# Optimization experiments

Hardware: AMD Instinct MI355X
Metric: run time of the kernel (lower is better)

Reference implementation:

```python
import jax, jax.numpy as jnp
import numpy as np

B, S, HID = 2, 2048, 1024
H, HKV, D = 8, 2, 256
G = H // HKV            # GQA group size = 4
RD = D // 4             # partial rotary dim = 64
BASE = 10000000.0
EPS = 1e-6


def _rmsnorm(x, w):
    # x: [..., D]; matches QwenRMSNorm (fp32 math)
    xf = x.astype(jnp.float32)
    var = jnp.mean(xf * xf, axis=-1, keepdims=True)
    return w * (xf * jax.lax.rsqrt(var + EPS)).astype(x.dtype)


def _rotate_half(x):
    h = x.shape[-1] // 2
    return jnp.concatenate([-x[..., h:], x[..., :h]], axis=-1)


def _rope_cos_sin(position_ids, dtype):
    inv_freq = 1.0 / (BASE ** (jnp.arange(0, RD, 2, dtype=jnp.float32) / RD))
    freqs = position_ids.astype(jnp.float32)[:, None] * inv_freq[None, :]  # [S, RD/2]
    emb = jnp.concatenate([freqs, freqs], axis=-1)                          # [S, RD]
    return jnp.cos(emb).astype(dtype)[None, None], jnp.sin(emb).astype(dtype)[None, None]


def setup_inputs() -> dict:
    key = jax.random.key(0)
    ks = jax.random.split(key, 8)
    sc = lambda fan_in: 1.0 / np.sqrt(fan_in)
    return {
        "hidden_states": jax.random.normal(ks[0], (B, S, HID), jnp.float32),
        "position_ids": jnp.arange(S, dtype=jnp.int32),
        "Wq": jax.random.normal(ks[1], (H * D * 2, HID), jnp.float32) * sc(HID),
        "Wk": jax.random.normal(ks[2], (HKV * D, HID), jnp.float32) * sc(HID),
        "Wv": jax.random.normal(ks[3], (HKV * D, HID), jnp.float32) * sc(HID),
        "Wo": jax.random.normal(ks[4], (HID, H * D), jnp.float32) * sc(H * D),
        "q_norm_w": jnp.ones((D,), jnp.float32),
        "k_norm_w": jnp.ones((D,), jnp.float32),
    }


def reference(hidden_states, position_ids, Wq, Wk, Wv, Wo, q_norm_w, k_norm_w):
    b, s, _ = hidden_states.shape
    q_and_gate = hidden_states @ Wq.T                      # [B,S,2*H*D]
    q = q_and_gate[..., : H * D]
    gate = q_and_gate[..., H * D :]
    k = hidden_states @ Wk.T                               # [B,S,HKV*D]
    v = hidden_states @ Wv.T

    q = _rmsnorm(q.reshape(b, s, H, D), q_norm_w).transpose(0, 2, 1, 3)    # [B,H,S,D]
    k = _rmsnorm(k.reshape(b, s, HKV, D), k_norm_w).transpose(0, 2, 1, 3)  # [B,HKV,S,D]
    v = v.reshape(b, s, HKV, D).transpose(0, 2, 1, 3)                       # [B,HKV,S,D]

    cos, sin = _rope_cos_sin(position_ids, q.dtype)        # [1,1,S,RD]
    q_rot, q_pass = q[..., :RD], q[..., RD:]
    k_rot, k_pass = k[..., :RD], k[..., RD:]
    q = jnp.concatenate([q_rot * cos + _rotate_half(q_rot) * sin, q_pass], axis=-1)
    k = jnp.concatenate([k_rot * cos + _rotate_half(k_rot) * sin, k_pass], axis=-1)

    # GQA: group q heads by kv head instead of repeat_interleave (same math)
    qg = q.reshape(b, HKV, G, s, D)
    scale = 1.0 / np.sqrt(D).astype(np.float32)
    scores = jnp.einsum('bhgqd,bhkd->bhgqk', qg, k) * scale  # [B,HKV,G,S,S]
    attn = jax.nn.softmax(scores, axis=-1)                   # NOTE: no causal mask (as in source)
    out = jnp.einsum('bhgqk,bhkd->bhgqd', attn, v)           # [B,HKV,G,S,D]
    out = out.reshape(b, H, s, D).transpose(0, 2, 1, 3).reshape(b, s, H * D)

    out = out * jax.nn.silu(gate)
    return out @ Wo.T
```

## Files before the change

### kernel.cpp

```cpp
#include <hip/hip_runtime.h>
#include <math.h>

typedef unsigned short u16;
typedef unsigned int   u32;
typedef __attribute__((ext_vector_type(4))) float f32x4;
typedef __attribute__((ext_vector_type(8))) short s16x8;
typedef __attribute__((ext_vector_type(4))) unsigned short u16x4;

#define B_N   2
#define S_N   2048
#define HID_N 1024
#define H_N   8
#define HKV_N 2
#define D_N   256
#define QKVW  5120

__device__ __forceinline__ u16 f2bf(float f) {
  union { float f; u32 u; } x; x.f = f;
  u32 r = x.u + 0x7FFFu + ((x.u >> 16) & 1u);
  return (u16)(r >> 16);
}
__device__ __forceinline__ float bf2f(u16 u) {
  union { u32 u; float f; } x; x.u = ((u32)u) << 16; return x.f;
}
__device__ __forceinline__ u32 pk_bf16(float lo, float hi) {
  u32 r;
  asm("v_cvt_pk_bf16_f32 %0, %1, %2" : "=v"(r) : "v"(lo), "v"(hi));
  return r;
}
__device__ __forceinline__ void gload_lds16(const u16* g, u16* l) {
  __builtin_amdgcn_global_load_lds((const __attribute__((address_space(1))) u32*)g,
                                   (__attribute__((address_space(3))) u32*)l, 16, 0, 0);
}

#define N4_HS 1048576
#define N4_WQ 1048576
#define N4_WK 131072
#define N4_WV 131072
#define N4_WO 524288
#define N4_TOT (N4_HS + N4_WQ + N4_WK + N4_WV + N4_WO)

__global__ __launch_bounds__(256)
void cast5_kernel(const float* __restrict__ hs, const float* __restrict__ wq,
                  const float* __restrict__ wk, const float* __restrict__ wv,
                  const float* __restrict__ wo, u16* __restrict__ hs_bf,
                  u16* __restrict__ wqkv_bf, u16* __restrict__ wo_bf) {
  int i = blockIdx.x * blockDim.x + threadIdx.x;
  const int stride = gridDim.x * blockDim.x;
  for (; i < N4_TOT; i += stride) {
    const float* src; u16* dst; int k;
    if (i < N4_HS)                         { src = hs; dst = hs_bf; k = i; }
    else if (i < N4_HS + N4_WQ)            { src = wq; dst = wqkv_bf; k = i - N4_HS; }
    else if (i < N4_HS + N4_WQ + N4_WK)    { src = wk; dst = wqkv_bf + 4194304; k = i - (N4_HS + N4_WQ); }
    else if (i < N4_TOT - N4_WO)           { src = wv; dst = wqkv_bf + 4718592; k = i - (N4_HS + N4_WQ + N4_WK); }
    else                                   { src = wo; dst = wo_bf; k = i - (N4_TOT - N4_WO); }
    float4 v = reinterpret_cast<const float4*>(src)[k];
    u16x4 o;
    o.x = f2bf(v.x); o.y = f2bf(v.y); o.z = f2bf(v.z); o.w = f2bf(v.w);
    reinterpret_cast<u16x4*>(dst)[k] = o;
  }
}

__global__ __launch_bounds__(256)
void trig_kernel(const int* __restrict__ pos, float* __restrict__ ct, float* __restrict__ st) {
  int i = blockIdx.x * blockDim.x + threadIdx.x;
  if (i >= S_N * 32) return;
  int s = i >> 5, j = i & 31;
  double inv = exp(-(double)j * (log(1.0e7) / 32.0));
  double ang = (double)pos[s] * inv;
  ct[i] = (float)cos(ang);
  st[i] = (float)sin(ang);
}

template <int OUT_BF16>
__global__ __launch_bounds__(256, 2)
void gemm_bt_kernel(const u16* __restrict__ A, const u16* __restrict__ Bw,
                    void* __restrict__ Cout, int M, int N, int K, int bn_per_x) {
  const int x = blockIdx.x & 7;
  const int i0 = blockIdx.x >> 3;
  const int bm = i0 / bn_per_x;
  const int bn = x * bn_per_x + (i0 - bm * bn_per_x);
  const int tid = threadIdx.x;
  const int lane = tid & 63;
  const int wr = tid >> 7;
  const int wc = (tid >> 6) & 1;
  __shared__ u16 sA[2][128 * 64];
  __shared__ u16 sB[2][128 * 64];
  f32x4 acc[4][4] = {};
  const u16* Ab = A + (size_t)(bm << 7) * K;
  const u16* Bb = Bw + (size_t)(bn << 7) * K;
  const int nkt = K >> 6;

  auto stage = [&](int buf, int kt) {
    const int k0 = kt << 6;
#pragma unroll
    for (int i = 0; i < 4; ++i) {
      const int L = i * 256 + tid;
      const int r = L >> 3, s = L & 7;
      gload_lds16(Ab + (size_t)r * K + k0 + ((s ^ (r & 7)) << 3), &sA[buf][L * 8]);
    }
#pragma unroll
    for (int i = 0; i < 4; ++i) {
      const int L = i * 256 + tid;
      const int r = L >> 3, s = L & 7;
      gload_lds16(Bb + (size_t)r * K + k0 + ((s ^ (r & 7)) << 3), &sB[buf][L * 8]);
    }
  };

  stage(0, 0);
  int cur = 0;
  const int ra = (wr << 6) + (lane & 15);
  const int rb = (wc << 6) + (lane & 15);
  const int l4 = (lane >> 4);
  const int sw = lane & 7;
  for (int kt = 0; kt < nkt; ++kt) {
    if (kt + 1 < nkt) {
      stage(cur ^ 1, kt + 1);
      asm volatile("s_waitcnt vmcnt(8)" ::: "memory");
    } else {
      asm volatile("s_waitcnt vmcnt(0)" ::: "memory");
    }
    __builtin_amdgcn_s_barrier();
    const u16* sa = sA[cur];
    const u16* sb = sB[cur];
#pragma unroll
    for (int kk = 0; kk < 2; ++kk) {
      const int sl = ((kk * 4 + l4) ^ sw) << 3;
      s16x8 af[4], bfr[4];
#pragma unroll
      for (int m = 0; m < 4; ++m)
        af[m] = *reinterpret_cast<const s16x8*>(sa + (ra + m * 16) * 64 + sl);
#pragma unroll
      for (int n = 0; n < 4; ++n)
        bfr[n] = *reinterpret_cast<const s16x8*>(sb + (rb + n * 16) * 64 + sl);
#pragma unroll
      for (int m = 0; m < 4; ++m)
#pragma unroll
        for (int n = 0; n < 4; ++n)
          acc[m][n] = __builtin_amdgcn_mfma_f32_16x16x32_bf16(af[m], bfr[n], acc[m][n], 0, 0, 0);
    }
    __builtin_amdgcn_s_barrier();
    cur ^= 1;
  }
  const int row0 = (bm << 7) + (wr << 6) + ((lane >> 4) << 2);
  const int col0 = (bn << 7) + (wc << 6) + (lane & 15);
#pragma unroll
  for (int m = 0; m < 4; ++m)
#pragma unroll
    for (int n = 0; n < 4; ++n)
#pragma unroll
      for (int j = 0; j < 4; ++j) {
        size_t idx = (size_t)(row0 + m * 16 + j) * N + col0 + n * 16;
        if (OUT_BF16) ((u16*)Cout)[idx] = f2bf(acc[m][n][j]);
        else          ((float*)Cout)[idx] = acc[m][n][j];
      }
}

__global__ __launch_bounds__(256)
void normrope_kernel(const u16* __restrict__ qkv, const float* __restrict__ qw,
                     const float* __restrict__ kw, const float* __restrict__ ct,
                     const float* __restrict__ st, u16* __restrict__ q_r,
                     u16* __restrict__ k_r) {
  const int lane = threadIdx.x & 63;
  const int row = blockIdx.x * 4 + (threadIdx.x >> 6);
  const int nq = B_N * S_N * H_N;
  const u16* src; u16* dst; const float* w;
  int s;
  if (row < nq) {
    int h = row & 7; int bs = row >> 3; s = bs & (S_N - 1); int b = bs >> 11;
    src = qkv + (size_t)(b * S_N + s) * QKVW + h * 256;
    dst = q_r + ((size_t)(b * H_N + h) * S_N + s) * 256;
    w = qw;
  } else {
    int r2 = row - nq;
    int h = r2 & 1; int bs = r2 >> 1; s = bs & (S_N - 1); int b = bs >> 11;
    src = qkv + (size_t)(b * S_N + s) * QKVW + 4096 + h * 256;
    dst = k_r + ((size_t)(b * HKV_N + h) * S_N + s) * 256;
    w = kw;
  }
  u16x4 xv = *reinterpret_cast<const u16x4*>(src + lane * 4);
  float x0 = bf2f(xv.x), x1 = bf2f(xv.y), x2 = bf2f(xv.z), x3 = bf2f(xv.w);
  float ss = x0 * x0 + x1 * x1 + x2 * x2 + x3 * x3;
#pragma unroll
  for (int off = 1; off < 64; off <<= 1) ss += __shfl_xor(ss, off);
  float rinv = rsqrtf(ss * (1.0f / 256.0f) + 1e-6f);
  float4 wv = *reinterpret_cast<const float4*>(w + lane * 4);
  float y[4] = { x0 * rinv * wv.x, x1 * rinv * wv.y, x2 * rinv * wv.z, x3 * rinv * wv.w };
  float p[4];
  p[0] = __shfl_xor(y[0], 8);
  p[1] = __shfl_xor(y[1], 8);
  p[2] = __shfl_xor(y[2], 8);
  p[3] = __shfl_xor(y[3], 8);
  if (lane < 16) {
    const float sgn = (lane < 8) ? -1.0f : 1.0f;
    const int jb = (lane * 4) & 31;
#pragma unroll
    for (int e = 0; e < 4; ++e) {
      float c = ct[(size_t)s * 32 + jb + e];
      float sn = st[(size_t)s * 32 + jb + e];
      y[e] = y[e] * c + sgn * p[e] * sn;
    }
  }
  u16x4 ov;
  ov.x = f2bf(y[0]); ov.y = f2bf(y[1]); ov.z = f2bf(y[2]); ov.w = f2bf(y[3]);
  *reinterpret_cast<u16x4*>(dst + lane * 4) = ov;
}

__global__ __launch_bounds__(256)
void vtrans_kernel(const u16* __restrict__ qkv, u16* __restrict__ vt) {
  const int bid = blockIdx.x;
  const int dt = bid & 3;
  const int stile = (bid >> 2) & 31;
  const int bh = bid >> 7;
  const int b = bh >> 1, kvh = bh & 1;
  __shared__ u16 tile[64][68];
  const int t = threadIdx.x;
  const u16* src = qkv + (size_t)(b * S_N + stile * 64) * QKVW + 4608 + kvh * 256 + dt * 64;
#pragma unroll
  for (int i = 0; i < 2; ++i) {
    int sl = i * 32 + (t >> 3);
    int d8 = (t & 7) * 8;
    s16x8 v = *reinterpret_cast<const s16x8*>(src + (size_t)sl * QKVW + d8);
    u16x4 lo = { (u16)v[0], (u16)v[1], (u16)v[2], (u16)v[3] };
    u16x4 hi = { (u16)v[4], (u16)v[5], (u16)v[6], (u16)v[7] };
    *reinterpret_cast<u16x4*>(&tile[sl][d8]) = lo;
    *reinterpret_cast<u16x4*>(&tile[sl][d8 + 4]) = hi;
  }
  __syncthreads();
#pragma unroll
  for (int i = 0; i < 2; ++i) {
    int dl = i * 32 + (t >> 3);
    int s8 = (t & 7) * 8;
    u16 tmp[8];
#pragma unroll
    for (int e = 0; e < 8; ++e) tmp[e] = tile[s8 + e][dl];
    u16x4 lo = { tmp[0], tmp[1], tmp[2], tmp[3] };
    u16x4 hi = { tmp[4], tmp[5], tmp[6], tmp[7] };
    u16* dstp = vt + ((size_t)(bh * 256 + dt * 64 + dl)) * S_N + stile * 64 + s8;
    *reinterpret_cast<u16x4*>(dstp) = lo;
    *reinterpret_cast<u16x4*>(dstp + 4) = hi;
  }
}

__global__ __launch_bounds__(512, 2)
void attn_kernel(const u16* __restrict__ q_r, const u16* __restrict__ k_r,
                 const u16* __restrict__ vt, const u16* __restrict__ qkv,
                 u16* __restrict__ act) {
  const int dd = blockIdx.x;
  const int xcd = dd & 7;
  const int idx = dd >> 3;
  const int combo = xcd >> 1;
  const int within = (xcd & 1) * 32 + idx;
  const int b = combo >> 1;
  const int kvh = combo & 1;
  const int h = kvh * 4 + (within >> 4);
  const int qt = within & 15;

  const int tid = threadIdx.x;
  const int lane = tid & 63;
  const int wv = tid >> 6;
  const int l15 = lane & 15;
  const int l4 = lane >> 4;

  __shared__ u16 sK[2][64 * 256];
  __shared__ u16 sVt[2][256 * 64];
  __shared__ u16 sP[8][16 * 64];

  const int q0 = qt * 128 + wv * 16;
  const u16* qb = q_r + ((size_t)(b * H_N + h) * S_N + q0) * 256;
  s16x8 qf[8];
#pragma unroll
  for (int kk = 0; kk < 8; ++kk)
    qf[kk] = *reinterpret_cast<const s16x8*>(qb + (size_t)l15 * 256 + kk * 32 + l4 * 8);

  f32x4 oacc[16] = {};
  float mrow = -1e30f;
  float lrow = 0.f;

  const u16* kbase = k_r + ((size_t)(b * HKV_N + kvh) * S_N) * 256;
  const u16* vbase = vt + ((size_t)(b * HKV_N + kvh) * 256) * S_N;

  const int krow_b = tid >> 5;
  const int kp = tid & 31;
  const int vrow_b = tid >> 3;
  const int vp = tid & 7;

  auto stageKV = [&](int buf, int step) {
    const int kv0 = step << 6;
#pragma unroll
    for (int i = 0; i < 4; ++i) {
      const int krow = i * 16 + krow_b;
      gload_lds16(kbase + (size_t)(kv0 + krow) * 256 + ((kp ^ (krow_b & 7)) << 3),
                  &sK[buf][i * 4096 + tid * 8]);
    }
#pragma unroll
    for (int i = 0; i < 4; ++i) {
      const int vrow = i * 64 + vrow_b;
      gload_lds16(vbase + (size_t)vrow * S_N + kv0 + ((vp ^ (vrow_b & 7)) << 3),
                  &sVt[buf][i * 4096 + tid * 8]);
    }
  };

  stageKV(0, 0);
  int cur = 0;
  const float scale = 0.0625f;
  const int sw = l15 & 7;
  const int swp = l15 & 14;
  for (int step = 0; step < 32; ++step) {
    asm volatile("s_waitcnt vmcnt(0)" ::: "memory");
    __builtin_amdgcn_s_barrier();
    if (step + 1 < 32) stageKV(cur ^ 1, step + 1);
    const u16* ktile = sK[cur];
    const u16* vtile = sVt[cur];

    f32x4 sacc[4] = {};
#pragma unroll
    for (int kk = 0; kk < 8; ++kk) {
      const int slot = kk * 4 + l4;
#pragma unroll
      for (int g = 0; g < 4; ++g) {
        s16x8 kf = *reinterpret_cast<const s16x8*>(
            ktile + (g * 16 + l15) * 256 + ((slot ^ sw) << 3));
        sacc[g] = __builtin_amdgcn_mfma_f32_16x16x32_bf16(kf, qf[kk], sacc[g], 0, 0, 0);
      }
    }

    float vmax = sacc[0][0];
#pragma unroll
    for (int g = 0; g < 4; ++g)
#pragma unroll
      for (int j = 0; j < 4; ++j) vmax = fmaxf(vmax, sacc[g][j]);
    vmax = fmaxf(vmax, __shfl_xor(vmax, 16));
    vmax = fmaxf(vmax, __shfl_xor(vmax, 32));
    if (__any(vmax > mrow)) {
      float mnew = fmaxf(mrow, vmax);
      float alpha = __expf((mrow - mnew) * scale);
      mrow = mnew;
      lrow *= alpha;
      float ab[4];
#pragma unroll
      for (int j = 0; j < 4; ++j) ab[j] = __shfl(alpha, l4 * 4 + j);
#pragma unroll
      for (int nf = 0; nf < 16; ++nf) {
        oacc[nf][0] *= ab[0]; oacc[nf][1] *= ab[1];
        oacc[nf][2] *= ab[2]; oacc[nf][3] *= ab[3];
      }
    }
    const float msc = mrow * scale;
    float p[16];
#pragma unroll
    for (int g = 0; g < 4; ++g)
#pragma unroll
      for (int j = 0; j < 4; ++j)
        p[g * 4 + j] = __expf(fmaf(sacc[g][j], scale, -msc));
    float r = ((p[0] + p[1]) + (p[2] + p[3])) + ((p[4] + p[5]) + (p[6] + p[7]))
            + ((p[8] + p[9]) + (p[10] + p[11])) + ((p[12] + p[13]) + (p[14] + p[15]));
    r += __shfl_xor(r, 16);
    r += __shfl_xor(r, 32);
    lrow += r;

    u16* pl = &sP[wv][0];
#pragma unroll
    for (int g = 0; g < 4; ++g) {
      u32 lo = pk_bf16(p[g * 4 + 0], p[g * 4 + 1]);
      u32 hi = pk_bf16(p[g * 4 + 2], p[g * 4 + 3]);
      union { u32 w[2]; u16x4 v; } u;
      u.w[0] = lo; u.w[1] = hi;
      *reinterpret_cast<u16x4*>(pl + l15 * 64 + (((g * 4 + l4) ^ swp) << 2)) = u.v;
    }
    asm volatile("s_waitcnt lgkmcnt(0)" ::: "memory");
    __builtin_amdgcn_sched_barrier(0);

#pragma unroll
    for (int c = 0; c < 2; ++c) {
      s16x8 paf = *reinterpret_cast<const s16x8*>(
          pl + l15 * 64 + (((c * 8 + l4 * 2) ^ swp) << 2));
#pragma unroll
      for (int nf = 0; nf < 16; ++nf) {
        s16x8 vf = *reinterpret_cast<const s16x8*>(
            vtile + (nf * 16 + l15) * 64 + (((c * 4 + l4) ^ sw) << 3));
        oacc[nf] = __builtin_amdgcn_mfma_f32_16x16x32_bf16(paf, vf, oacc[nf], 0, 0, 0);
      }
    }
    cur ^= 1;
  }

  float invl = 1.0f / lrow;
  float ib[4];
#pragma unroll
  for (int j = 0; j < 4; ++j) ib[j] = __shfl(invl, l4 * 4 + j);
#pragma unroll
  for (int nf = 0; nf < 16; ++nf) {
#pragma unroll
    for (int j = 0; j < 4; ++j) {
      const int srow = q0 + l4 * 4 + j;
      const int d = nf * 16 + l15;
      float o = oacc[nf][j] * ib[j];
      float g = bf2f(qkv[(size_t)(b * S_N + srow) * QKVW + 2048 + h * 256 + d]);
      float sg = g / (1.0f + __expf(-g));
      act[(size_t)(b * S_N + srow) * 2048 + h * 256 + d] = f2bf(o * sg);
    }
  }
}

extern "C" void kernel_launch(void* const* d_in, const int* in_sizes, int n_in,
                              void* d_out, int out_size, void* d_ws, size_t ws_size,
                              hipStream_t stream) {
  const float* hs  = (const float*)d_in[0];
  const int*   pos = (const int*)d_in[1];
  const float* Wq  = (const float*)d_in[2];
  const float* Wk  = (const float*)d_in[3];
  const float* Wv  = (const float*)d_in[4];
  const float* Wo  = (const float*)d_in[5];
  const float* qw  = (const float*)d_in[6];
  const float* kw  = (const float*)d_in[7];
  float* out = (float*)d_out;

  char* w8 = (char*)d_ws;
  u16* hs_bf   = (u16*)(w8);
  u16* wqkv_bf = (u16*)(w8 + 8388608);
  u16* wo_bf   = (u16*)(w8 + 18874368);
  u16* qkv_raw = (u16*)(w8 + 23068672);
  u16* q_r     = (u16*)(w8 + 65011712);
  u16* k_r     = (u16*)(w8 + 81788928);
  u16* vt      = (u16*)(w8 + 85983232);
  u16* act     = (u16*)(w8 + 90177536);
  float* cost  = (float*)(w8 + 106954752);
  float* sint  = (float*)(w8 + 107216896);

  cast5_kernel<<<2048, 256, 0, stream>>>(hs, Wq, Wk, Wv, Wo, hs_bf, wqkv_bf, wo_bf);

  trig_kernel<<<(S_N * 32) / 256, 256, 0, stream>>>(pos, cost, sint);

  gemm_bt_kernel<1><<<1280, 256, 0, stream>>>(hs_bf, wqkv_bf, (void*)qkv_raw,
                                              4096, 5120, 1024, 5);

  normrope_kernel<<<(B_N * S_N * (H_N + HKV_N)) / 4, 256, 0, stream>>>(
      qkv_raw, qw, kw, cost, sint, q_r, k_r);
  vtrans_kernel<<<512, 256, 0, stream>>>(qkv_raw, vt);

  attn_kernel<<<256, 512, 0, stream>>>(q_r, k_r, vt, qkv_raw, act);

  gemm_bt_kernel<0><<<256, 256, 0, stream>>>(act, wo_bf, (void*)out,
                                             4096, 1024, 2048, 1);
}
```

Baseline: 220.8 us.

## Share K/V tiles across GQA heads and split KV range between wave groups

Result: slower. 244.6 us (+10.8%).

```diff
diff --git a/kernel.cpp b/kernel.cpp
--- a/kernel.cpp
+++ b/kernel.cpp
@@ -250,54 +250,60 @@
   const int xcd = dd & 7;
   const int idx = dd >> 3;
   const int combo = xcd >> 1;
-  const int within = (xcd & 1) * 32 + idx;
+  const int qt = (xcd & 1) * 32 + idx;
   const int b = combo >> 1;
   const int kvh = combo & 1;
-  const int h = kvh * 4 + (within >> 4);
-  const int qt = within & 15;
 
   const int tid = threadIdx.x;
   const int lane = tid & 63;
   const int wv = tid >> 6;
+  const int grp = wv >> 2;
+  const int hw = wv & 3;
+  const int h = kvh * 4 + hw;
   const int l15 = lane & 15;
   const int l4 = lane >> 4;
 
-  __shared__ u16 sK[2][64 * 256];
-  __shared__ u16 sVt[2][256 * 64];
-  __shared__ u16 sP[8][16 * 64];
-
-  const int q0 = qt * 128 + wv * 16;
+  __shared__ u16 smem[74752];
+  u16* sKg = smem + grp * 16384;
+  u16* sVg = smem + 32768 + grp * 16384;
+  u16* sPw = smem + 65536 + wv * 1024;
+  float* sml = (float*)(smem + 73728);
+
+  const int q0 = qt * 32;
   const u16* qb = q_r + ((size_t)(b * H_N + h) * S_N + q0) * 256;
-  s16x8 qf[8];
-#pragma unroll
-  for (int kk = 0; kk < 8; ++kk)
-    qf[kk] = *reinterpret_cast<const s16x8*>(qb + (size_t)l15 * 256 + kk * 32 + l4 * 8);
-
-  f32x4 oacc[16] = {};
-  float mrow = -1e30f;
-  float lrow = 0.f;
+  s16x8 qf[2][8];
+#pragma unroll
+  for (int rg = 0; rg < 2; ++rg)
+#pragma unroll
+    for (int kk = 0; kk < 8; ++kk)
+      qf[rg][kk] = *reinterpret_cast<const s16x8*>(
+          qb + (size_t)(rg * 16 + l15) * 256 + kk * 32 + l4 * 8);
+
+  f32x4 oacc[2][16] = {};
+  float mrow[2] = { -1e30f, -1e30f };
+  float lrow[2] = { 0.f, 0.f };
 
   const u16* kbase = k_r + ((size_t)(b * HKV_N + kvh) * S_N) * 256;
   const u16* vbase = vt + ((size_t)(b * HKV_N + kvh) * 256) * S_N;
-
-  const int krow_b = tid >> 5;
-  const int kp = tid & 31;
-  const int vrow_b = tid >> 3;
-  const int vp = tid & 7;
+  const int gt = tid & 255;
 
   auto stageKV = [&](int buf, int step) {
-    const int kv0 = step << 6;
+    const int kv0 = grp * 1024 + (step << 5);
+    u16* kb = sKg + buf * 8192;
+    u16* vb = sVg + buf * 8192;
 #pragma unroll
     for (int i = 0; i < 4; ++i) {
-      const int krow = i * 16 + krow_b;
-      gload_lds16(kbase + (size_t)(kv0 + krow) * 256 + ((kp ^ (krow_b & 7)) << 3),
-                  &sK[buf][i * 4096 + tid * 8]);
+      const int L = i * 256 + gt;
+      const int krow = L >> 5, ks = L & 31;
+      gload_lds16(kbase + (size_t)(kv0 + krow) * 256 + ((ks ^ (krow & 7)) << 3),
+                  kb + L * 8);
     }
 #pragma unroll
     for (int i = 0; i < 4; ++i) {
-      const int vrow = i * 64 + vrow_b;
-      gload_lds16(vbase + (size_t)vrow * S_N + kv0 + ((vp ^ (vrow_b & 7)) << 3),
-                  &sVt[buf][i * 4096 + tid * 8]);
+      const int L = i * 256 + gt;
+      const int vrow = L >> 2, vs = L & 3;
+      gload_lds16(vbase + (size_t)vrow * S_N + kv0 + ((vs ^ (vrow & 3)) << 3),
+                  vb + L * 8);
     }
   };
 
@@ -305,101 +311,161 @@
   int cur = 0;
   const float scale = 0.0625f;
   const int sw = l15 & 7;
-  const int swp = l15 & 14;
+  const int sw3 = l15 & 3;
   for (int step = 0; step < 32; ++step) {
     asm volatile("s_waitcnt vmcnt(0)" ::: "memory");
     __builtin_amdgcn_s_barrier();
     if (step + 1 < 32) stageKV(cur ^ 1, step + 1);
-    const u16* ktile = sK[cur];
-    const u16* vtile = sVt[cur];
-
-    f32x4 sacc[4] = {};
+    const u16* ktile = sKg + cur * 8192;
+    const u16* vtile = sVg + cur * 8192;
+
+    f32x4 sacc[2][2] = {};
 #pragma unroll
     for (int kk = 0; kk < 8; ++kk) {
       const int slot = kk * 4 + l4;
 #pragma unroll
-      for (int g = 0; g < 4; ++g) {
+      for (int g = 0; g < 2; ++g) {
         s16x8 kf = *reinterpret_cast<const s16x8*>(
             ktile + (g * 16 + l15) * 256 + ((slot ^ sw) << 3));
-        sacc[g] = __builtin_amdgcn_mfma_f32_16x16x32_bf16(kf, qf[kk], sacc[g], 0, 0, 0);
+        sacc[0][g] = __builtin_amdgcn_mfma_f32_16x16x32_bf16(kf, qf[0][kk], sacc[0][g], 0, 0, 0);
+        sacc[1][g] = __builtin_amdgcn_mfma_f32_16x16x32_bf16(kf, qf[1][kk], sacc[1][g], 0, 0, 0);
       }
     }
 
-    float vmax = sacc[0][0];
-#pragma unroll
-    for (int g = 0; g < 4; ++g)
-#pragma unroll
-      for (int j = 0; j < 4; ++j) vmax = fmaxf(vmax, sacc[g][j]);
-    vmax = fmaxf(vmax, __shfl_xor(vmax, 16));
-    vmax = fmaxf(vmax, __shfl_xor(vmax, 32));
-    if (__any(vmax > mrow)) {
-      float mnew = fmaxf(mrow, vmax);
-      float alpha = __expf((mrow - mnew) * scale);
-      mrow = mnew;
-      lrow *= alpha;
-      float ab[4];
-#pragma unroll
-      for (int j = 0; j < 4; ++j) ab[j] = __shfl(alpha, l4 * 4 + j);
-#pragma unroll
-      for (int nf = 0; nf < 16; ++nf) {
-        oacc[nf][0] *= ab[0]; oacc[nf][1] *= ab[1];
-        oacc[nf][2] *= ab[2]; oacc[nf][3] *= ab[3];
+    float vmax[2];
+#pragma unroll
+    for (int rg = 0; rg < 2; ++rg) {
+      float v = fmaxf(fmaxf(fmaxf(sacc[rg][0][0], sacc[rg][0][1]),
+                            fmaxf(sacc[rg][0][2], sacc[rg][0][3])),
+                      fmaxf(fmaxf(sacc[rg][1][0], sacc[rg][1][1]),
+                            fmaxf(sacc[rg][1][2], sacc[rg][1][3])));
+      v = fmaxf(v, __shfl_xor(v, 16));
+      v = fmaxf(v, __shfl_xor(v, 32));
+      vmax[rg] = v;
+    }
+    if (__any(fmaxf(vmax[0] - mrow[0], vmax[1] - mrow[1]) > 0.0f)) {
+      float alpha[2];
+#pragma unroll
+      for (int rg = 0; rg < 2; ++rg) {
+        float mnew = fmaxf(mrow[rg], vmax[rg]);
+        alpha[rg] = __expf((mrow[rg] - mnew) * scale);
+        mrow[rg] = mnew;
+        lrow[rg] *= alpha[rg];
       }
-    }
-    const float msc = mrow * scale;
-    float p[16];
-#pragma unroll
-    for (int g = 0; g < 4; ++g)
-#pragma unroll
-      for (int j = 0; j < 4; ++j)
-        p[g * 4 + j] = __expf(fmaf(sacc[g][j], scale, -msc));
-    float r = ((p[0] + p[1]) + (p[2] + p[3])) + ((p[4] + p[5]) + (p[6] + p[7]))
-            + ((p[8] + p[9]) + (p[10] + p[11])) + ((p[12] + p[13]) + (p[14] + p[15]));
-    r += __shfl_xor(r, 16);
-    r += __shfl_xor(r, 32);
-    lrow += r;
-
-    u16* pl = &sP[wv][0];
-#pragma unroll
-    for (int g = 0; g < 4; ++g) {
-      u32 lo = pk_bf16(p[g * 4 + 0], p[g * 4 + 1]);
-      u32 hi = pk_bf16(p[g * 4 + 2], p[g * 4 + 3]);
-      union { u32 w[2]; u16x4 v; } u;
-      u.w[0] = lo; u.w[1] = hi;
-      *reinterpret_cast<u16x4*>(pl + l15 * 64 + (((g * 4 + l4) ^ swp) << 2)) = u.v;
+      float ab[2][4];
+#pragma unroll
+      for (int rg = 0; rg < 2; ++rg)
+#pragma unroll
+        for (int j = 0; j < 4; ++j) ab[rg][j] = __shfl(alpha[rg], l4 * 4 + j);
+#pragma unroll
+      for (int nf = 0; nf < 16; ++nf)
+#pragma unroll
+        for (int rg = 0; rg < 2; ++rg) {
+          oacc[rg][nf][0] *= ab[rg][0]; oacc[rg][nf][1] *= ab[rg][1];
+          oacc[rg][nf][2] *= ab[rg][2]; oacc[rg][nf][3] *= ab[rg][3];
+        }
+    }
+    float p[2][8];
+#pragma unroll
+    for (int rg = 0; rg < 2; ++rg) {
+      const float msc = mrow[rg] * scale;
+#pragma unroll
+      for (int g = 0; g < 2; ++g)
+#pragma unroll
+        for (int j = 0; j < 4; ++j)
+          p[rg][g * 4 + j] = __expf(fmaf(sacc[rg][g][j], scale, -msc));
+      float r = ((p[rg][0] + p[rg][1]) + (p[rg][2] + p[rg][3]))
+              + ((p[rg][4] + p[rg][5]) + (p[rg][6] + p[rg][7]));
+      r += __shfl_xor(r, 16);
+      r += __shfl_xor(r, 32);
+      lrow[rg] += r;
+    }
+
+#pragma unroll
+    for (int rg = 0; rg < 2; ++rg) {
+      const int rowoff = (rg * 16 + l15) * 32;
+#pragma unroll
+      for (int g = 0; g < 2; ++g) {
+        u32 a = pk_bf16(p[rg][g * 4 + 0], p[rg][g * 4 + 1]);
+        u32 c = pk_bf16(p[rg][g * 4 + 2], p[rg][g * 4 + 3]);
+        union { u32 w[2]; u16x4 v; } u;
+        u.w[0] = a; u.w[1] = c;
+        *reinterpret_cast<u16x4*>(
+            sPw + rowoff + (((g * 2 + (l4 >> 1)) ^ sw3) << 3) + ((l4 & 1) << 2)) = u.v;
+      }
     }
     asm volatile("s_waitcnt lgkmcnt(0)" ::: "memory");
     __builtin_amdgcn_sched_barrier(0);
 
-#pragma unroll
-    for (int c = 0; c < 2; ++c) {
-      s16x8 paf = *reinterpret_cast<const s16x8*>(
-          pl + l15 * 64 + (((c * 8 + l4 * 2) ^ swp) << 2));
-#pragma unroll
-      for (int nf = 0; nf < 16; ++nf) {
-        s16x8 vf = *reinterpret_cast<const s16x8*>(
-            vtile + (nf * 16 + l15) * 64 + (((c * 4 + l4) ^ sw) << 3));
-        oacc[nf] = __builtin_amdgcn_mfma_f32_16x16x32_bf16(paf, vf, oacc[nf], 0, 0, 0);
+    s16x8 paf[2];
+#pragma unroll
+    for (int rg = 0; rg < 2; ++rg)
+      paf[rg] = *reinterpret_cast<const s16x8*>(
+          sPw + (rg * 16 + l15) * 32 + ((l4 ^ sw3) << 3));
+#pragma unroll
+    for (int nf = 0; nf < 16; ++nf) {
+      s16x8 vf = *reinterpret_cast<const s16x8*>(
+          vtile + (nf * 16 + l15) * 32 + ((l4 ^ sw3) << 3));
+      oacc[0][nf] = __builtin_amdgcn_mfma_f32_16x16x32_bf16(paf[0], vf, oacc[0][nf], 0, 0, 0);
+      oacc[1][nf] = __builtin_amdgcn_mfma_f32_16x16x32_bf16(paf[1], vf, oacc[1][nf], 0, 0, 0);
+    }
+    cur ^= 1;
+  }
+
+  __syncthreads();
+  if (l4 == 0) {
+    sml[wv * 64 + l15 * 2]            = mrow[0];
+    sml[wv * 64 + l15 * 2 + 1]        = lrow[0];
+    sml[wv * 64 + (16 + l15) * 2]     = mrow[1];
+    sml[wv * 64 + (16 + l15) * 2 + 1] = lrow[1];
+  }
+  float* mergeO = (float*)smem;
+  if (grp == 1) {
+#pragma unroll
+    for (int rg = 0; rg < 2; ++rg)
+#pragma unroll
+      for (int nf = 0; nf < 16; ++nf)
+#pragma unroll
+        for (int j = 0; j < 4; ++j) {
+          const int q = rg * 16 + l4 * 4 + j;
+          const int d = nf * 16 + l15;
+          mergeO[(hw * 32 + q) * 260 + d] = oacc[rg][nf][j];
+        }
+  }
+  __syncthreads();
+  if (grp == 0) {
+    float W0[2][4], W1[2][4];
+#pragma unroll
+    for (int rg = 0; rg < 2; ++rg)
+#pragma unroll
+      for (int j = 0; j < 4; ++j) {
+        const int q = rg * 16 + l4 * 4 + j;
+        const float m0 = sml[hw * 64 + q * 2];
+        const float l0 = sml[hw * 64 + q * 2 + 1];
+        const float m1 = sml[(4 + hw) * 64 + q * 2];
+        const float l1 = sml[(4 + hw) * 64 + q * 2 + 1];
+        const float M = fmaxf(m0, m1);
+        const float w0 = __expf((m0 - M) * scale);
+        const float w1 = __expf((m1 - M) * scale);
+        const float inv = 1.0f / (l0 * w0 + l1 * w1);
+        W0[rg][j] = w0 * inv;
+        W1[rg][j] = w1 * inv;
       }
-    }
-    cur ^= 1;
-  }
-
-  float invl = 1.0f / lrow;
-  float ib[4];
-#pragma unroll
-  for (int j = 0; j < 4; ++j) ib[j] = __shfl(invl, l4 * 4 + j);
-#pragma unroll
-  for (int nf = 0; nf < 16; ++nf) {
-#pragma unroll
-    for (int j = 0; j < 4; ++j) {
-      const int srow = q0 + l4 * 4 + j;
-      const int d = nf * 16 + l15;
-      float o = oacc[nf][j] * ib[j];
-      float g = bf2f(qkv[(size_t)(b * S_N + srow) * QKVW + 2048 + h * 256 + d]);
-      float sg = g / (1.0f + __expf(-g));
-      act[(size_t)(b * S_N + srow) * 2048 + h * 256 + d] = f2bf(o * sg);
-    }
+#pragma unroll
+    for (int rg = 0; rg < 2; ++rg)
+#pragma unroll
+      for (int nf = 0; nf < 16; ++nf)
+#pragma unroll
+        for (int j = 0; j < 4; ++j) {
+          const int q = rg * 16 + l4 * 4 + j;
+          const int d = nf * 16 + l15;
+          const int srow = q0 + q;
+          float o = oacc[rg][nf][j] * W0[rg][j]
+                  + mergeO[(hw * 32 + q) * 260 + d] * W1[rg][j];
+          float g = bf2f(qkv[(size_t)(b * S_N + srow) * QKVW + 2048 + h * 256 + d]);
+          float sg = g / (1.0f + __expf(-g));
+          act[(size_t)(b * S_N + srow) * 2048 + h * 256 + d] = f2bf(o * sg);
+        }
   }
 }
 
```

## Software-pipeline attention loop to overlap next QK with current PV

Applied to the files above, without the earlier changes.

Result: no change. 219.5 us, median of 3 (-0.6%).

```diff
diff --git a/kernel.cpp b/kernel.cpp
--- a/kernel.cpp
+++ b/kernel.cpp
@@ -264,7 +264,7 @@
 
   __shared__ u16 sK[2][64 * 256];
   __shared__ u16 sVt[2][256 * 64];
-  __shared__ u16 sP[8][16 * 64];
+  __shared__ u16 sP[8][2][16 * 64];
 
   const int q0 = qt * 128 + wv * 16;
   const u16* qb = q_r + ((size_t)(b * H_N + h) * S_N + q0) * 256;
@@ -285,7 +285,7 @@
   const int vrow_b = tid >> 3;
   const int vp = tid & 7;
 
-  auto stageKV = [&](int buf, int step) {
+  auto stageK = [&](int buf, int step) {
     const int kv0 = step << 6;
 #pragma unroll
     for (int i = 0; i < 4; ++i) {
@@ -293,6 +293,9 @@
       gload_lds16(kbase + (size_t)(kv0 + krow) * 256 + ((kp ^ (krow_b & 7)) << 3),
                   &sK[buf][i * 4096 + tid * 8]);
     }
+  };
+  auto stageV = [&](int buf, int step) {
+    const int kv0 = step << 6;
 #pragma unroll
     for (int i = 0; i < 4; ++i) {
       const int vrow = i * 64 + vrow_b;
@@ -301,19 +304,11 @@
     }
   };
 
-  stageKV(0, 0);
-  int cur = 0;
   const float scale = 0.0625f;
   const int sw = l15 & 7;
   const int swp = l15 & 14;
-  for (int step = 0; step < 32; ++step) {
-    asm volatile("s_waitcnt vmcnt(0)" ::: "memory");
-    __builtin_amdgcn_s_barrier();
-    if (step + 1 < 32) stageKV(cur ^ 1, step + 1);
-    const u16* ktile = sK[cur];
-    const u16* vtile = sVt[cur];
-
-    f32x4 sacc[4] = {};
+
+  auto computeQK = [&](const u16* ktile, f32x4* sacc) {
 #pragma unroll
     for (int kk = 0; kk < 8; ++kk) {
       const int slot = kk * 4 + l4;
@@ -324,7 +319,10 @@
         sacc[g] = __builtin_amdgcn_mfma_f32_16x16x32_bf16(kf, qf[kk], sacc[g], 0, 0, 0);
       }
     }
-
+  };
+  float alphaNext = 1.0f;
+  int doRescale = 0;
+  auto softmaxPack = [&](f32x4* sacc, int pb) {
     float vmax = sacc[0][0];
 #pragma unroll
     for (int g = 0; g < 4; ++g)
@@ -332,19 +330,14 @@
       for (int j = 0; j < 4; ++j) vmax = fmaxf(vmax, sacc[g][j]);
     vmax = fmaxf(vmax, __shfl_xor(vmax, 16));
     vmax = fmaxf(vmax, __shfl_xor(vmax, 32));
-    if (__any(vmax > mrow)) {
+    doRescale = __any(vmax > mrow) ? 1 : 0;
+    if (doRescale) {
       float mnew = fmaxf(mrow, vmax);
-      float alpha = __expf((mrow - mnew) * scale);
+      alphaNext = __expf((mrow - mnew) * scale);
       mrow = mnew;
-      lrow *= alpha;
-      float ab[4];
-#pragma unroll
-      for (int j = 0; j < 4; ++j) ab[j] = __shfl(alpha, l4 * 4 + j);
-#pragma unroll
-      for (int nf = 0; nf < 16; ++nf) {
-        oacc[nf][0] *= ab[0]; oacc[nf][1] *= ab[1];
-        oacc[nf][2] *= ab[2]; oacc[nf][3] *= ab[3];
-      }
+      lrow *= alphaNext;
+    } else {
+      alphaNext = 1.0f;
     }
     const float msc = mrow * scale;
     float p[16];
@@ -358,8 +351,7 @@
     r += __shfl_xor(r, 16);
     r += __shfl_xor(r, 32);
     lrow += r;
-
-    u16* pl = &sP[wv][0];
+    u16* pl = &sP[wv][pb][0];
 #pragma unroll
     for (int g = 0; g < 4; ++g) {
       u32 lo = pk_bf16(p[g * 4 + 0], p[g * 4 + 1]);
@@ -368,9 +360,39 @@
       u.w[0] = lo; u.w[1] = hi;
       *reinterpret_cast<u16x4*>(pl + l15 * 64 + (((g * 4 + l4) ^ swp) << 2)) = u.v;
     }
-    asm volatile("s_waitcnt lgkmcnt(0)" ::: "memory");
-    __builtin_amdgcn_sched_barrier(0);
-
+  };
+
+  stageK(0, 0);
+  stageV(0, 0);
+  stageK(1, 1);
+  asm volatile("s_waitcnt vmcnt(0)" ::: "memory");
+  __builtin_amdgcn_s_barrier();
+  {
+    f32x4 sacc[4] = {};
+    computeQK(sK[0], sacc);
+    softmaxPack(sacc, 0);
+  }
+
+  for (int t = 0; t < 32; ++t) {
+    asm volatile("s_waitcnt vmcnt(0)" ::: "memory");
+    __builtin_amdgcn_s_barrier();
+    if (t + 2 < 32) stageK(t & 1, t + 2);
+    if (t + 1 < 32) stageV((t + 1) & 1, t + 1);
+
+    if (doRescale) {
+      float ab[4];
+#pragma unroll
+      for (int j = 0; j < 4; ++j) ab[j] = __shfl(alphaNext, l4 * 4 + j);
+#pragma unroll
+      for (int nf = 0; nf < 16; ++nf) {
+        oacc[nf][0] *= ab[0]; oacc[nf][1] *= ab[1];
+        oacc[nf][2] *= ab[2]; oacc[nf][3] *= ab[3];
+      }
+    }
+
+    __builtin_amdgcn_s_setprio(1);
+    const u16* pl = &sP[wv][t & 1][0];
+    const u16* vtile = sVt[t & 1];
 #pragma unroll
     for (int c = 0; c < 2; ++c) {
       s16x8 paf = *reinterpret_cast<const s16x8*>(
@@ -382,7 +404,11 @@
         oacc[nf] = __builtin_amdgcn_mfma_f32_16x16x32_bf16(paf, vf, oacc[nf], 0, 0, 0);
       }
     }
-    cur ^= 1;
+    f32x4 sacc[4] = {};
+    if (t + 1 < 32) computeQK(sK[(t + 1) & 1], sacc);
+    __builtin_amdgcn_s_setprio(0);
+
+    if (t + 1 < 32) softmaxPack(sacc, (t + 1) & 1);
   }
 
   float invl = 1.0f / lrow;
```

## Split attention KV range across wave pairs with 32x32 MFMA and merge partials

Applied to the files above, without the earlier changes.

Result: slower. 367.4 us (+66.4%).

```diff
diff --git a/kernel.cpp b/kernel.cpp
--- a/kernel.cpp
+++ b/kernel.cpp
@@ -4,6 +4,7 @@
 typedef unsigned short u16;
 typedef unsigned int   u32;
 typedef __attribute__((ext_vector_type(4))) float f32x4;
+typedef __attribute__((ext_vector_type(16))) float f32x16;
 typedef __attribute__((ext_vector_type(8))) short s16x8;
 typedef __attribute__((ext_vector_type(4))) unsigned short u16x4;
 
@@ -242,7 +243,7 @@
   }
 }
 
-__global__ __launch_bounds__(512, 2)
+__global__ __launch_bounds__(256, 2)
 void attn_kernel(const u16* __restrict__ q_r, const u16* __restrict__ k_r,
                  const u16* __restrict__ vt, const u16* __restrict__ qkv,
                  u16* __restrict__ act) {
@@ -250,155 +251,173 @@
   const int xcd = dd & 7;
   const int idx = dd >> 3;
   const int combo = xcd >> 1;
-  const int within = (xcd & 1) * 32 + idx;
+  const int within = (xcd & 1) * 64 + idx;
   const int b = combo >> 1;
   const int kvh = combo & 1;
-  const int h = kvh * 4 + (within >> 4);
-  const int qt = within & 15;
+  const int h = kvh * 4 + (within >> 5);
+  const int qtile = within & 31;
 
   const int tid = threadIdx.x;
   const int lane = tid & 63;
-  const int wv = tid >> 6;
-  const int l15 = lane & 15;
-  const int l4 = lane >> 4;
-
-  __shared__ u16 sK[2][64 * 256];
-  __shared__ u16 sVt[2][256 * 64];
-  __shared__ u16 sP[8][16 * 64];
-
-  const int q0 = qt * 128 + wv * 16;
+  const int w = tid >> 6;
+  const int half = w >> 1;
+  const int l31 = lane & 31;
+  const int l5 = lane >> 5;
+
+  __shared__ u16 smem[36864];
+  u16* sK = smem + half * 8192;
+  u16* sV = smem + 16384 + half * 8192;
+  u16* sP = smem + 32768 + w * 1024;
+
+  const int q0 = qtile * 64 + (w & 1) * 32;
   const u16* qb = q_r + ((size_t)(b * H_N + h) * S_N + q0) * 256;
-  s16x8 qf[8];
-#pragma unroll
-  for (int kk = 0; kk < 8; ++kk)
-    qf[kk] = *reinterpret_cast<const s16x8*>(qb + (size_t)l15 * 256 + kk * 32 + l4 * 8);
-
-  f32x4 oacc[16] = {};
-  float mrow = -1e30f;
-  float lrow = 0.f;
-
-  const u16* kbase = k_r + ((size_t)(b * HKV_N + kvh) * S_N) * 256;
-  const u16* vbase = vt + ((size_t)(b * HKV_N + kvh) * 256) * S_N;
-
-  const int krow_b = tid >> 5;
-  const int kp = tid & 31;
-  const int vrow_b = tid >> 3;
-  const int vp = tid & 7;
-
-  auto stageKV = [&](int buf, int step) {
-    const int kv0 = step << 6;
-#pragma unroll
-    for (int i = 0; i < 4; ++i) {
-      const int krow = i * 16 + krow_b;
-      gload_lds16(kbase + (size_t)(kv0 + krow) * 256 + ((kp ^ (krow_b & 7)) << 3),
-                  &sK[buf][i * 4096 + tid * 8]);
-    }
-#pragma unroll
-    for (int i = 0; i < 4; ++i) {
-      const int vrow = i * 64 + vrow_b;
-      gload_lds16(vbase + (size_t)vrow * S_N + kv0 + ((vp ^ (vrow_b & 7)) << 3),
-                  &sVt[buf][i * 4096 + tid * 8]);
+  s16x8 qf[16];
+#pragma unroll
+  for (int ks = 0; ks < 16; ++ks)
+    qf[ks] = *reinterpret_cast<const s16x8*>(qb + (size_t)l31 * 256 + ks * 16 + l5 * 8);
+
+  f32x16 oacc[8] = {};
+  float mrow = -1e30f, lrow = 0.f;
+
+  const u16* kbase = k_r + (size_t)(b * HKV_N + kvh) * S_N * 256;
+  const u16* vbase = vt + (size_t)(b * HKV_N + kvh) * 256 * S_N;
+  const int lt = tid & 127;
+
+  auto stage = [&](int step) {
+    const int kv0 = half * 1024 + (step << 5);
+#pragma unroll
+    for (int i = 0; i < 8; ++i) {
+      const int L = i * 128 + lt;
+      const int kv = L >> 5, s = L & 31;
+      gload_lds16(kbase + (size_t)(kv0 + kv) * 256 + ((s ^ kv) << 3), sK + L * 8);
+    }
+#pragma unroll
+    for (int i = 0; i < 8; ++i) {
+      const int L = i * 128 + lt;
+      const int d = L >> 2, s = L & 3;
+      gload_lds16(vbase + (size_t)d * S_N + kv0 + ((s ^ (d & 3)) << 3), sV + L * 8);
     }
   };
 
-  stageKV(0, 0);
-  int cur = 0;
   const float scale = 0.0625f;
-  const int sw = l15 & 7;
-  const int swp = l15 & 14;
-  for (int step = 0; step < 32; ++step) {
-    asm volatile("s_waitcnt vmcnt(0)" ::: "memory");
-    __builtin_amdgcn_s_barrier();
-    if (step + 1 < 32) stageKV(cur ^ 1, step + 1);
-    const u16* ktile = sK[cur];
-    const u16* vtile = sVt[cur];
-
-    f32x4 sacc[4] = {};
-#pragma unroll
-    for (int kk = 0; kk < 8; ++kk) {
-      const int slot = kk * 4 + l4;
-#pragma unroll
-      for (int g = 0; g < 4; ++g) {
-        s16x8 kf = *reinterpret_cast<const s16x8*>(
-            ktile + (g * 16 + l15) * 256 + ((slot ^ sw) << 3));
-        sacc[g] = __builtin_amdgcn_mfma_f32_16x16x32_bf16(kf, qf[kk], sacc[g], 0, 0, 0);
-      }
-    }
-
-    float vmax = sacc[0][0];
-#pragma unroll
-    for (int g = 0; g < 4; ++g)
-#pragma unroll
-      for (int j = 0; j < 4; ++j) vmax = fmaxf(vmax, sacc[g][j]);
-    vmax = fmaxf(vmax, __shfl_xor(vmax, 16));
+  stage(0);
+  asm volatile("s_waitcnt vmcnt(0)" ::: "memory");
+  __builtin_amdgcn_s_barrier();
+
+  for (int t = 0; t < 32; ++t) {
+    f32x16 sacc = {};
+    __builtin_amdgcn_s_setprio(1);
+#pragma unroll
+    for (int ks = 0; ks < 16; ++ks) {
+      s16x8 kf = *reinterpret_cast<const s16x8*>(
+          sK + l31 * 256 + (((2 * ks + l5) ^ l31) << 3));
+      sacc = __builtin_amdgcn_mfma_f32_32x32x16_bf16(kf, qf[ks], sacc, 0, 0, 0);
+    }
+    __builtin_amdgcn_s_setprio(0);
+
+    float vmax = sacc[0];
+#pragma unroll
+    for (int r = 1; r < 16; ++r) vmax = fmaxf(vmax, sacc[r]);
     vmax = fmaxf(vmax, __shfl_xor(vmax, 32));
     if (__any(vmax > mrow)) {
       float mnew = fmaxf(mrow, vmax);
       float alpha = __expf((mrow - mnew) * scale);
       mrow = mnew;
       lrow *= alpha;
-      float ab[4];
-#pragma unroll
-      for (int j = 0; j < 4; ++j) ab[j] = __shfl(alpha, l4 * 4 + j);
-#pragma unroll
-      for (int nf = 0; nf < 16; ++nf) {
-        oacc[nf][0] *= ab[0]; oacc[nf][1] *= ab[1];
-        oacc[nf][2] *= ab[2]; oacc[nf][3] *= ab[3];
+#pragma unroll
+      for (int r = 0; r < 16; ++r) {
+        const int qreg = (r & 3) + 8 * (r >> 2) + 4 * l5;
+        float ab = __shfl(alpha, qreg);
+#pragma unroll
+        for (int dt = 0; dt < 8; ++dt) oacc[dt][r] *= ab;
       }
     }
     const float msc = mrow * scale;
     float p[16];
 #pragma unroll
-    for (int g = 0; g < 4; ++g)
-#pragma unroll
-      for (int j = 0; j < 4; ++j)
-        p[g * 4 + j] = __expf(fmaf(sacc[g][j], scale, -msc));
-    float r = ((p[0] + p[1]) + (p[2] + p[3])) + ((p[4] + p[5]) + (p[6] + p[7]))
-            + ((p[8] + p[9]) + (p[10] + p[11])) + ((p[12] + p[13]) + (p[14] + p[15]));
-    r += __shfl_xor(r, 16);
-    r += __shfl_xor(r, 32);
-    lrow += r;
-
-    u16* pl = &sP[wv][0];
+    for (int r = 0; r < 16; ++r) p[r] = __expf(fmaf(sacc[r], scale, -msc));
+    float rs = ((p[0] + p[1]) + (p[2] + p[3])) + ((p[4] + p[5]) + (p[6] + p[7]))
+             + ((p[8] + p[9]) + (p[10] + p[11])) + ((p[12] + p[13]) + (p[14] + p[15]));
+    rs += __shfl_xor(rs, 32);
+    lrow += rs;
+
 #pragma unroll
     for (int g = 0; g < 4; ++g) {
-      u32 lo = pk_bf16(p[g * 4 + 0], p[g * 4 + 1]);
-      u32 hi = pk_bf16(p[g * 4 + 2], p[g * 4 + 3]);
-      union { u32 w[2]; u16x4 v; } u;
-      u.w[0] = lo; u.w[1] = hi;
-      *reinterpret_cast<u16x4*>(pl + l15 * 64 + (((g * 4 + l4) ^ swp) << 2)) = u.v;
+      u32 lo = pk_bf16(p[4 * g + 0], p[4 * g + 1]);
+      u32 hi = pk_bf16(p[4 * g + 2], p[4 * g + 3]);
+      union { u32 wd[2]; u16x4 v; } u;
+      u.wd[0] = lo; u.wd[1] = hi;
+      const int slot8 = (2 * g + l5) ^ ((l31 & 3) << 1);
+      *reinterpret_cast<u16x4*>(sP + l31 * 32 + slot8 * 4) = u.v;
     }
     asm volatile("s_waitcnt lgkmcnt(0)" ::: "memory");
     __builtin_amdgcn_sched_barrier(0);
 
-#pragma unroll
-    for (int c = 0; c < 2; ++c) {
-      s16x8 paf = *reinterpret_cast<const s16x8*>(
-          pl + l15 * 64 + (((c * 8 + l4 * 2) ^ swp) << 2));
-#pragma unroll
-      for (int nf = 0; nf < 16; ++nf) {
+    s16x8 pa[2];
+#pragma unroll
+    for (int ks = 0; ks < 2; ++ks)
+      pa[ks] = *reinterpret_cast<const s16x8*>(
+          sP + l31 * 32 + (((4 * ks + 2 * l5) ^ ((l31 & 3) << 1)) << 2));
+    __builtin_amdgcn_s_setprio(1);
+#pragma unroll
+    for (int dt = 0; dt < 8; ++dt) {
+      const int drow = dt * 32 + l31;
+#pragma unroll
+      for (int ks = 0; ks < 2; ++ks) {
         s16x8 vf = *reinterpret_cast<const s16x8*>(
-            vtile + (nf * 16 + l15) * 64 + (((c * 4 + l4) ^ sw) << 3));
-        oacc[nf] = __builtin_amdgcn_mfma_f32_16x16x32_bf16(paf, vf, oacc[nf], 0, 0, 0);
+            sV + drow * 32 + (((4 * ks + 2 * l5) ^ ((l31 & 3) << 1)) << 2));
+        oacc[dt] = __builtin_amdgcn_mfma_f32_32x32x16_bf16(pa[ks], vf, oacc[dt], 0, 0, 0);
       }
     }
-    cur ^= 1;
-  }
-
-  float invl = 1.0f / lrow;
-  float ib[4];
-#pragma unroll
-  for (int j = 0; j < 4; ++j) ib[j] = __shfl(invl, l4 * 4 + j);
-#pragma unroll
-  for (int nf = 0; nf < 16; ++nf) {
-#pragma unroll
-    for (int j = 0; j < 4; ++j) {
-      const int srow = q0 + l4 * 4 + j;
-      const int d = nf * 16 + l15;
-      float o = oacc[nf][j] * ib[j];
-      float g = bf2f(qkv[(size_t)(b * S_N + srow) * QKVW + 2048 + h * 256 + d]);
-      float sg = g / (1.0f + __expf(-g));
-      act[(size_t)(b * S_N + srow) * 2048 + h * 256 + d] = f2bf(o * sg);
+    __builtin_amdgcn_s_setprio(0);
+
+    __builtin_amdgcn_s_barrier();
+    if (t + 1 < 32) {
+      stage(t + 1);
+      asm volatile("s_waitcnt vmcnt(0)" ::: "memory");
+      __builtin_amdgcn_s_barrier();
+    }
+  }
+
+  __syncthreads();
+  float* mergeO = (float*)smem;
+  float* mlb = (float*)(smem + 33280);
+  if (lane < 32) {
+    float2 v2 = { mrow, lrow };
+    *reinterpret_cast<float2*>(mlb + (w * 32 + l31) * 2) = v2;
+  }
+  if (half == 1) {
+#pragma unroll
+    for (int dt = 0; dt < 8; ++dt)
+#pragma unroll
+      for (int r = 0; r < 16; ++r) {
+        const int qreg = (r & 3) + 8 * (r >> 2) + 4 * l5;
+        mergeO[((w & 1) * 32 + qreg) * 260 + dt * 32 + l31] = oacc[dt][r];
+      }
+  }
+  __syncthreads();
+  if (half == 0) {
+    const float2 ml1 = *reinterpret_cast<const float2*>(mlb + ((w + 2) * 32 + l31) * 2);
+    const float M = fmaxf(mrow, ml1.x);
+    const float e0 = __expf((mrow - M) * scale);
+    const float e1 = __expf((ml1.x - M) * scale);
+    const float inv = 1.0f / (lrow * e0 + ml1.y * e1);
+    const float w0n = e0 * inv, w1n = e1 * inv;
+#pragma unroll
+    for (int r = 0; r < 16; ++r) {
+      const int qreg = (r & 3) + 8 * (r >> 2) + 4 * l5;
+      const float W0 = __shfl(w0n, qreg);
+      const float W1 = __shfl(w1n, qreg);
+      const int qloc = (w & 1) * 32 + qreg;
+      const int srow = qtile * 64 + qloc;
+#pragma unroll
+      for (int dt = 0; dt < 8; ++dt) {
+        const int d = dt * 32 + l31;
+        float o = oacc[dt][r] * W0 + mergeO[qloc * 260 + d] * W1;
+        float g = bf2f(qkv[(size_t)(b * S_N + srow) * QKVW + 2048 + h * 256 + d]);
+        float sg = g / (1.0f + __expf(-g));
+        act[(size_t)(b * S_N + srow) * 2048 + h * 256 + d] = f2bf(o * sg);
+      }
     }
   }
 }
@@ -439,7 +458,7 @@
       qkv_raw, qw, kw, cost, sint, q_r, k_r);
   vtrans_kernel<<<512, 256, 0, stream>>>(qkv_raw, vt);
 
-  attn_kernel<<<256, 512, 0, stream>>>(q_r, k_r, vt, qkv_raw, act);
+  attn_kernel<<<512, 256, 0, stream>>>(q_r, k_r, vt, qkv_raw, act);
 
   gemm_bt_kernel<0><<<256, 256, 0, stream>>>(act, wo_bf, (void*)out,
                                              4096, 1024, 2048, 1);
```
